# Kernel optimization log

Measured on AMD Instinct MI355X. Metric: run time of the kernel, lower is better.

The kernel has to match this reference:

```python
import jax, jax.numpy as jnp
import numpy as np

CANVAS = 28
MARGIN = 2
HALF = CANVAS / 2.0          # 14
SCALE = CANVAS / 2.0 - MARGIN  # 12
P = 2        # num_paths
SEG = 4      # final segments
T = 8        # curve samples per bezier segment
AA = 2       # 2x2 = 4 anti-alias subsamples per pixel


def _lin(x, w, b):
    return x @ w + b


def _render(cp, widths, alphas):
    """diffvg-style rasterizer.
    cp: [B,P,S,4,2] cubic bezier control points, widths/alphas: [B,P].
    Returns [B,1,H,W] image over white background (paths paint dark).
    """
    B = cp.shape[0]
    t = jnp.linspace(0.0, 1.0, T)
    mt = 1.0 - t
    basis = jnp.stack([mt**3, 3*mt**2*t, 3*mt*t**2, t**3], axis=1)  # [T,4]
    pts = jnp.einsum('tk,bpskd->bpstd', basis, cp)                   # [B,P,S,T,2]
    q = pts.reshape(B, P, SEG * T, 2)                                # polyline [B,P,M,2]

    # 2x2 subpixel sample grid over the canvas
    Nf = CANVAS * AA
    c = (jnp.arange(Nf, dtype=jnp.float32) + 0.5) / AA               # fine coords
    sy, sx = jnp.meshgrid(c, c, indexing='ij')
    s = jnp.stack([sx.ravel(), sy.ravel()], axis=-1)                 # [Ns,2] (x,y)

    # stroke coverage: distance from each sample to nearest curve sample
    qq = jnp.sum(q * q, axis=-1)                                     # [B,P,M]
    ss = jnp.sum(s * s, axis=-1)                                     # [Ns]
    cr = jnp.einsum('bpmd,nd->bpmn', q, s)                           # [B,P,M,Ns]
    d2 = jnp.maximum(qq[..., None] + ss - 2.0 * cr, 0.0)
    dist = jnp.sqrt(jnp.min(d2, axis=2))                             # [B,P,Ns]
    stroke = jnp.clip(widths[..., None] * 0.5 + 0.5 - dist, 0.0, 1.0)

    # fill coverage: even-odd crossing number on the closed polyline
    qn = jnp.roll(q, -1, axis=2)
    x0, y0 = q[..., 0], q[..., 1]
    x1, y1 = qn[..., 0], qn[..., 1]
    syf, sxf = s[:, 1], s[:, 0]
    crossing_band = (y0[..., None] > syf) != (y1[..., None] > syf)   # [B,P,M,Ns]
    te = (syf - y0[..., None]) / (y1[..., None] - y0[..., None] + 1e-8)
    xint = x0[..., None] + te * (x1 - x0)[..., None]
    ncross = jnp.sum((crossing_band & (sxf < xint)).astype(jnp.int32), axis=2)
    inside = (ncross % 2).astype(dist.dtype)                         # [B,P,Ns]

    cov = jnp.maximum(inside, stroke)
    img = jnp.prod(1.0 - alphas[..., None] * cov, axis=1)            # composite over paths, bg=1
    img = img.reshape(B, CANVAS, AA, CANVAS, AA).mean(axis=(2, 4))   # AA resolve
    return img[:, None]                                              # [B,1,H,W]


def setup_inputs() -> dict:
    key = jax.random.key(0)
    ks = jax.random.split(key, 16)
    def W(k, i, o):
        return jax.random.normal(k, (i, o), jnp.float32) / np.sqrt(i).astype(np.float32)
    B = 128
    return {
        'x': jax.random.uniform(ks[0], (B, 1, 28, 28), jnp.float32),
        'eps': jax.random.normal(ks[1], (B, 64), jnp.float32),
        'enc_w1': W(ks[2], 784, 256), 'enc_b1': jnp.zeros((256,), jnp.float32),
        'enc_w2': W(ks[3], 256, 256), 'enc_b2': jnp.zeros((256,), jnp.float32),
        'mu_w': W(ks[4], 256, 64), 'mu_b': jnp.zeros((64,), jnp.float32),
        'lv_w': W(ks[5], 256, 64), 'lv_b': jnp.zeros((64,), jnp.float32),
        'dec_w1': W(ks[6], 64, 512), 'dec_b1': jnp.zeros((512,), jnp.float32),
        'dec_w2': W(ks[7], 512, 512), 'dec_b2': jnp.zeros((512,), jnp.float32),
        'cp_w': W(ks[8], 512, 28), 'cp_b': jnp.zeros((28,), jnp.float32),
        'ref_w1': W(ks[9], 92, 512), 'ref_b1': jnp.zeros((512,), jnp.float32),
        'ref_w2': W(ks[10], 512, 52), 'ref_b2': jnp.zeros((52,), jnp.float32),
        'wd_w': W(ks[11], 512, 2), 'wd_b': jnp.zeros((2,), jnp.float32),
        'al_w': W(ks[12], 512, 2), 'al_b': jnp.zeros((2,), jnp.float32),
    }


def reference(x, eps, enc_w1, enc_b1, enc_w2, enc_b2, mu_w, mu_b, lv_w, lv_b,
              dec_w1, dec_b1, dec_w2, dec_b2, cp_w, cp_b,
              ref_w1, ref_b1, ref_w2, ref_b2, wd_w, wd_b, al_w, al_b):
    B = x.shape[0]
    # encoder
    h = jax.nn.leaky_relu(_lin(x.reshape(B, -1), enc_w1, enc_b1), 0.2)
    h = jax.nn.leaky_relu(_lin(h, enc_w2, enc_b2), 0.2)
    mu = _lin(h, mu_w, mu_b)
    logvar = _lin(h, lv_w, lv_b)
    z = mu + eps * jnp.exp(0.5 * logvar)
    # hierarchical decoder
    h2 = jax.nn.selu(_lin(jax.nn.selu(_lin(z, dec_w1, dec_b1)), dec_w2, dec_b2))
    coarse = jnp.tanh(_lin(h2, cp_w, cp_b)).reshape(B, P, 7, 2) * SCALE + HALF
    pts_norm = (coarse - HALF) / SCALE
    h_in = jnp.concatenate([z, pts_norm.reshape(B, -1)], axis=-1)
    refined = jnp.tanh(_lin(jax.nn.selu(_lin(h_in, ref_w1, ref_b1)), ref_w2, ref_b2))
    points = refined.reshape(B, P, 13, 2) * SCALE + HALF
    seg_idx = 3 * jnp.arange(SEG)[:, None] + jnp.arange(4)[None, :]  # [S,4]
    control_points = points[:, :, seg_idx, :]                         # [B,P,S,4,2]
    widths = jax.nn.sigmoid(_lin(h2, wd_w, wd_b)) * 2.0 + 1.0
    alphas = jax.nn.sigmoid(_lin(h2, al_w, al_b))
    rendered = 1.0 - _render(control_points, widths, alphas)          # white digit on black
    return (rendered, mu, logvar, control_points, widths, alphas)
```

## Files before the change

kernel.cpp:

```cpp
#include <hip/hip_runtime.h>
#include <math.h>


#define O_MU  100352
#define O_LV  108544
#define O_CP  116736
#define O_WD  124928
#define O_AL  125184

#define W_H1   0
#define W_HE   32768
#define W_MUT  65536
#define W_LVT  73728
#define W_D1   81920
#define W_H2   147456
#define W_PN   212992
#define W_R1   216576
#define W_PT   282112
#define W_WA   288768

__device__ __forceinline__ float leaky(float x) { return x >= 0.f ? x : 0.2f * x; }
__device__ __forceinline__ float seluf(float x) {
    const float s = 1.0507009873554805f, a = 1.6732632423543772f;
    return x > 0.f ? s * x : s * (a * expm1f(x));
}
__device__ __forceinline__ float sigm(float x) { return 1.f / (1.f + expf(-x)); }

__global__ __launch_bounds__(512)
void enc1_k(const float* __restrict__ x, const float* __restrict__ w,
            const float* __restrict__ b, float* __restrict__ outT) {
    __shared__ float part[8][64];
    const int j = blockIdx.x >> 1, h = blockIdx.x & 1;
    const int tid = threadIdx.x, lane = tid & 63, ks = tid >> 6;
    const int r = h * 64 + lane;
    const float* __restrict__ xr = x + r * 784;
    float acc = 0.f;
    const int k0 = ks * 98;
#pragma unroll 7
    for (int i = 0; i < 98; i++)
        acc = fmaf(xr[k0 + i], w[(k0 + i) * 256 + j], acc);
    part[ks][lane] = acc;
    __syncthreads();
    if (tid < 64) {
        float s = b[j];
#pragma unroll
        for (int q = 0; q < 8; q++) s += part[q][tid];
        outT[j * 128 + h * 64 + tid] = leaky(s);
    }
}

__global__ __launch_bounds__(512)
void enc2_k(const float* __restrict__ inT, const float* __restrict__ w,
            const float* __restrict__ b, float* __restrict__ outT) {
    __shared__ float part[8][64];
    const int j = blockIdx.x >> 1, h = blockIdx.x & 1;
    const int tid = threadIdx.x, lane = tid & 63, ks = tid >> 6;
    const int r = h * 64 + lane;
    float acc = 0.f;
    const int k0 = ks * 32;
#pragma unroll 8
    for (int i = 0; i < 32; i++)
        acc = fmaf(inT[(k0 + i) * 128 + r], w[(k0 + i) * 256 + j], acc);
    part[ks][lane] = acc;
    __syncthreads();
    if (tid < 64) {
        float s = b[j];
#pragma unroll
        for (int q = 0; q < 8; q++) s += part[q][tid];
        outT[j * 128 + h * 64 + tid] = leaky(s);
    }
}

__global__ __launch_bounds__(512)
void mulv_k(const float* __restrict__ heT,
            const float* __restrict__ mu_w, const float* __restrict__ mu_b,
            const float* __restrict__ lv_w, const float* __restrict__ lv_b,
            float* __restrict__ muT, float* __restrict__ lvT,
            float* __restrict__ out) {
    __shared__ float part[8][64];
    const int meta = blockIdx.x >> 1, h = blockIdx.x & 1;
    const int head = meta >> 6, col = meta & 63;
    const float* __restrict__ w = head ? lv_w : mu_w;
    const int tid = threadIdx.x, lane = tid & 63, ks = tid >> 6;
    const int r = h * 64 + lane;
    float acc = 0.f;
    const int k0 = ks * 32;
#pragma unroll 8
    for (int i = 0; i < 32; i++)
        acc = fmaf(heT[(k0 + i) * 128 + r], w[(k0 + i) * 64 + col], acc);
    part[ks][lane] = acc;
    __syncthreads();
    if (tid < 64) {
        float s = (head ? lv_b : mu_b)[col];
#pragma unroll
        for (int q = 0; q < 8; q++) s += part[q][tid];
        const int rr = h * 64 + tid;
        (head ? lvT : muT)[col * 128 + rr] = s;
        out[(head ? O_LV : O_MU) + rr * 64 + col] = s;
    }
}

__global__ __launch_bounds__(512)
void dec1_k(const float* __restrict__ muT, const float* __restrict__ lvT,
            const float* __restrict__ eps, const float* __restrict__ w,
            const float* __restrict__ b, float* __restrict__ outT) {
    __shared__ float part[8][2][64];
    const int j0 = (blockIdx.x >> 1) * 2, h = blockIdx.x & 1;
    const int tid = threadIdx.x, lane = tid & 63, ks = tid >> 6;
    const int r = h * 64 + lane;
    float a0 = 0.f, a1 = 0.f;
    const int k0 = ks * 8;
#pragma unroll
    for (int i = 0; i < 8; i++) {
        const int k = k0 + i;
        float zv = fmaf(eps[r * 64 + k], expf(0.5f * lvT[k * 128 + r]), muT[k * 128 + r]);
        a0 = fmaf(zv, w[k * 512 + j0],     a0);
        a1 = fmaf(zv, w[k * 512 + j0 + 1], a1);
    }
    part[ks][0][lane] = a0; part[ks][1][lane] = a1;
    __syncthreads();
    if (tid < 128) {
        const int c = tid >> 6, ll = tid & 63;
        float s = b[j0 + c];
#pragma unroll
        for (int q = 0; q < 8; q++) s += part[q][c][ll];
        outT[(j0 + c) * 128 + h * 64 + ll] = seluf(s);
    }
}

__global__ __launch_bounds__(512)
void dec2_k(const float* __restrict__ inT, const float* __restrict__ w,
            const float* __restrict__ b, float* __restrict__ outT) {
    __shared__ float part[8][2][64];
    const int j0 = (blockIdx.x >> 1) * 2, h = blockIdx.x & 1;
    const int tid = threadIdx.x, lane = tid & 63, ks = tid >> 6;
    const int r = h * 64 + lane;
    float a0 = 0.f, a1 = 0.f;
    const int k0 = ks * 64;
#pragma unroll 4
    for (int i = 0; i < 64; i++) {
        const float v = inT[(k0 + i) * 128 + r];
        a0 = fmaf(v, w[(k0 + i) * 512 + j0],     a0);
        a1 = fmaf(v, w[(k0 + i) * 512 + j0 + 1], a1);
    }
    part[ks][0][lane] = a0; part[ks][1][lane] = a1;
    __syncthreads();
    if (tid < 128) {
        const int c = tid >> 6, ll = tid & 63;
        float s = b[j0 + c];
#pragma unroll
        for (int q = 0; q < 8; q++) s += part[q][c][ll];
        outT[(j0 + c) * 128 + h * 64 + ll] = seluf(s);
    }
}

__global__ __launch_bounds__(512)
void heads_k(const float* __restrict__ h2T,
             const float* __restrict__ cp_w, const float* __restrict__ cp_b,
             const float* __restrict__ wd_w, const float* __restrict__ wd_b,
             const float* __restrict__ al_w, const float* __restrict__ al_b,
             float* __restrict__ pnT, float* __restrict__ waT,
             float* __restrict__ out) {
    __shared__ float part[8][64];
    const int j = blockIdx.x >> 1, h = blockIdx.x & 1;
    const float* __restrict__ w; int ldw, col;
    if (j < 28)      { w = cp_w; ldw = 28; col = j; }
    else if (j < 30) { w = wd_w; ldw = 2;  col = j - 28; }
    else             { w = al_w; ldw = 2;  col = j - 30; }
    const int tid = threadIdx.x, lane = tid & 63, ks = tid >> 6;
    const int r = h * 64 + lane;
    float acc = 0.f;
    const int k0 = ks * 64;
#pragma unroll 8
    for (int i = 0; i < 64; i++)
        acc = fmaf(h2T[(k0 + i) * 128 + r], w[(k0 + i) * ldw + col], acc);
    part[ks][lane] = acc;
    __syncthreads();
    if (tid < 64) {
        float s = 0.f;
#pragma unroll
        for (int q = 0; q < 8; q++) s += part[q][tid];
        const int rr = h * 64 + tid;
        if (j < 28) {
            pnT[j * 128 + rr] = tanhf(s + cp_b[col]);
        } else if (j < 30) {
            float v = fmaf(sigm(s + wd_b[col]), 2.f, 1.f);
            out[O_WD + rr * 2 + col] = v; waT[col * 128 + rr] = v;
        } else {
            float v = sigm(s + al_b[col]);
            out[O_AL + rr * 2 + col] = v; waT[(2 + col) * 128 + rr] = v;
        }
    }
}

__global__ __launch_bounds__(512)
void ref1_k(const float* __restrict__ muT, const float* __restrict__ lvT,
            const float* __restrict__ eps, const float* __restrict__ pnT,
            const float* __restrict__ w, const float* __restrict__ b,
            float* __restrict__ outT) {
    __shared__ float part[8][2][64];
    const int j0 = (blockIdx.x >> 1) * 2, h = blockIdx.x & 1;
    const int tid = threadIdx.x, lane = tid & 63, ks = tid >> 6;
    const int r = h * 64 + lane;
    float a0 = 0.f, a1 = 0.f;
#pragma unroll
    for (int i = 0; i < 12; i++) {
        const int k = ks * 12 + i;
        if (k < 92) {
            float v = (k < 64)
                ? fmaf(eps[r * 64 + k], expf(0.5f * lvT[k * 128 + r]), muT[k * 128 + r])
                : pnT[(k - 64) * 128 + r];
            a0 = fmaf(v, w[k * 512 + j0],     a0);
            a1 = fmaf(v, w[k * 512 + j0 + 1], a1);
        }
    }
    part[ks][0][lane] = a0; part[ks][1][lane] = a1;
    __syncthreads();
    if (tid < 128) {
        const int c = tid >> 6, ll = tid & 63;
        float s = b[j0 + c];
#pragma unroll
        for (int q = 0; q < 8; q++) s += part[q][c][ll];
        outT[(j0 + c) * 128 + h * 64 + ll] = seluf(s);
    }
}

__global__ __launch_bounds__(512)
void ref2_k(const float* __restrict__ r1T, const float* __restrict__ w,
            const float* __restrict__ b, float* __restrict__ PT) {
    __shared__ float part[8][64];
    const int j = blockIdx.x >> 1, h = blockIdx.x & 1;
    const int tid = threadIdx.x, lane = tid & 63, ks = tid >> 6;
    const int r = h * 64 + lane;
    float acc = 0.f;
    const int k0 = ks * 64;
#pragma unroll 8
    for (int i = 0; i < 64; i++)
        acc = fmaf(r1T[(k0 + i) * 128 + r], w[(k0 + i) * 52 + j], acc);
    part[ks][lane] = acc;
    __syncthreads();
    if (tid < 64) {
        float s = b[j];
#pragma unroll
        for (int q = 0; q < 8; q++) s += part[q][tid];
        PT[j * 128 + h * 64 + tid] = fmaf(tanhf(s), 12.f, 14.f);
    }
}

__global__ __launch_bounds__(512)
void raster_k(const float* __restrict__ PT, const float* __restrict__ waT,
              float* __restrict__ out) {
    __shared__ float sP[56];
    __shared__ float sWA[4];
    __shared__ float sQ[128];
    const int bid = blockIdx.x;
    const int row = bid / 7, chunk = bid - row * 7;
    const int tid = threadIdx.x;
    if (tid < 52) sP[tid] = PT[tid * 128 + row];
    if (tid >= 64 && tid < 68) sWA[tid - 64] = waT[(tid - 64) * 128 + row];
    __syncthreads();
    if (chunk == 0 && tid < 64) {
        const int idx = tid, p = idx >> 5, rest = idx & 31;
        const int s = rest >> 3, kk = (rest >> 1) & 3, d = idx & 1;
        out[O_CP + row * 64 + idx] = sP[p * 26 + (3 * s + kk) * 2 + d];
    }
    if (tid < 128) {
        const int idx = tid, p = idx >> 6, s = (idx >> 4) & 3, ti = (idx >> 1) & 7, d = idx & 1;
        const float t = (float)ti / 7.0f, mt = 1.0f - t;
        const float c0 = mt * mt * mt, c1 = 3.f * mt * mt * t;
        const float c2 = 3.f * mt * t * t, c3 = t * t * t;
        const float* base = sP + p * 26 + 6 * s + d;
        sQ[idx] = c0 * base[0] + c1 * base[2] + c2 * base[4] + c3 * base[6];
    }
    __syncthreads();
    if (tid < 448) {
        const int pixel = chunk * 112 + (tid >> 2), sub = tid & 3;
        const int py = pixel / 28, px = pixel - py * 28;
        const float sy = ((float)(2 * py + (sub >> 1)) + 0.5f) * 0.5f;
        const float sx = ((float)(2 * px + (sub & 1)) + 0.5f) * 0.5f;
        const float2* __restrict__ sQ2 = (const float2*)sQ;
        float img = 1.0f;
#pragma unroll
        for (int p = 0; p < 2; p++) {
            float dmin2 = 1e30f;
            int cnt = 0;
            float2 cur = sQ2[p * 32];
            bool bp = cur.y > sy;
#pragma unroll
            for (int m = 0; m < 32; m++) {
                float2 nxt = sQ2[p * 32 + ((m + 1) & 31)];
                float dx = sx - cur.x;
                float dy = sy - cur.y;
                dmin2 = fminf(dmin2, fmaf(dx, dx, dy * dy));
                bool bn = nxt.y > sy;
                float den = nxt.y - cur.y + 1e-8f;
                float lhs = dx * den;
                float rhs = dy * (nxt.x - cur.x);
                if ((bp != bn) && ((lhs < rhs) == (den > 0.0f))) cnt++;
                cur = nxt;
                bp = bn;
            }
            float dist = sqrtf(dmin2);
            float stroke = fminf(fmaxf(fmaf(sWA[p], 0.5f, 0.5f) - dist, 0.f), 1.f);
            float cov = fmaxf((float)(cnt & 1), stroke);
            img *= fmaf(-sWA[2 + p], cov, 1.0f);
        }
        img += __shfl_xor(img, 1);
        img += __shfl_xor(img, 2);
        if (sub == 0) out[row * 784 + pixel] = 1.0f - 0.25f * img;
    }
}

extern "C" void kernel_launch(void* const* d_in, const int* in_sizes, int n_in,
                              void* d_out, int out_size, void* d_ws, size_t ws_size,
                              hipStream_t stream) {
    const float* x      = (const float*)d_in[0];
    const float* eps    = (const float*)d_in[1];
    const float* enc_w1 = (const float*)d_in[2];
    const float* enc_b1 = (const float*)d_in[3];
    const float* enc_w2 = (const float*)d_in[4];
    const float* enc_b2 = (const float*)d_in[5];
    const float* mu_w   = (const float*)d_in[6];
    const float* mu_b   = (const float*)d_in[7];
    const float* lv_w   = (const float*)d_in[8];
    const float* lv_b   = (const float*)d_in[9];
    const float* dec_w1 = (const float*)d_in[10];
    const float* dec_b1 = (const float*)d_in[11];
    const float* dec_w2 = (const float*)d_in[12];
    const float* dec_b2 = (const float*)d_in[13];
    const float* cp_w   = (const float*)d_in[14];
    const float* cp_b   = (const float*)d_in[15];
    const float* ref_w1 = (const float*)d_in[16];
    const float* ref_b1 = (const float*)d_in[17];
    const float* ref_w2 = (const float*)d_in[18];
    const float* ref_b2 = (const float*)d_in[19];
    const float* wd_w   = (const float*)d_in[20];
    const float* wd_b   = (const float*)d_in[21];
    const float* al_w   = (const float*)d_in[22];
    const float* al_b   = (const float*)d_in[23];

    float* out = (float*)d_out;
    float* ws  = (float*)d_ws;

    enc1_k <<<512, 512, 0, stream>>>(x, enc_w1, enc_b1, ws + W_H1);
    enc2_k <<<512, 512, 0, stream>>>(ws + W_H1, enc_w2, enc_b2, ws + W_HE);
    mulv_k <<<256, 512, 0, stream>>>(ws + W_HE, mu_w, mu_b, lv_w, lv_b,
                                     ws + W_MUT, ws + W_LVT, out);
    dec1_k <<<512, 512, 0, stream>>>(ws + W_MUT, ws + W_LVT, eps,
                                     dec_w1, dec_b1, ws + W_D1);
    dec2_k <<<512, 512, 0, stream>>>(ws + W_D1, dec_w2, dec_b2, ws + W_H2);
    heads_k<<<64, 512, 0, stream>>>(ws + W_H2, cp_w, cp_b, wd_w, wd_b, al_w, al_b,
                                    ws + W_PN, ws + W_WA, out);
    ref1_k <<<512, 512, 0, stream>>>(ws + W_MUT, ws + W_LVT, eps, ws + W_PN,
                                     ref_w1, ref_b1, ws + W_R1);
    ref2_k <<<104, 512, 0, stream>>>(ws + W_R1, ref_w2, ref_b2, ws + W_PT);
    raster_k<<<896, 512, 0, stream>>>(ws + W_PT, ws + W_WA, out);
}
```

Baseline: 190.0 us.

## Fuse whole VAE pipeline into one cooperative kernel with grid syncs

Replaces the nine separate layer and raster launches with a single cooperative kernel of 256 blocks that uses grid-wide syncs between layers. It also splits the refine layer so the z-dependent part is computed while the heads run, and it touches later-layer weights early to warm the cache. The aim is to remove per-launch overhead and inter-kernel gaps. In exchange it runs fewer blocks per stage and adds the cost of each grid barrier.

Result: slower. 469.8 us (+147.3%).

```diff
diff --git a/kernel.cpp b/kernel.cpp
--- a/kernel.cpp
+++ b/kernel.cpp
@@ -1,5 +1,8 @@
 #include <hip/hip_runtime.h>
+#include <hip/hip_cooperative_groups.h>
 #include <math.h>
+
+namespace cg = cooperative_groups;
 
 
 #define O_MU  100352
@@ -15,9 +18,10 @@
 #define W_D1   81920
 #define W_H2   147456
 #define W_PN   212992
-#define W_R1   216576
-#define W_PT   282112
-#define W_WA   288768
+#define W_R1Z  216576
+#define W_R1   282112
+#define W_PT   347648
+#define W_WA   354304
 
 __device__ __forceinline__ float leaky(float x) { return x >= 0.f ? x : 0.2f * x; }
 __device__ __forceinline__ float seluf(float x) {
@@ -27,287 +31,300 @@
 __device__ __forceinline__ float sigm(float x) { return 1.f / (1.f + expf(-x)); }
 
 __global__ __launch_bounds__(512)
-void enc1_k(const float* __restrict__ x, const float* __restrict__ w,
-            const float* __restrict__ b, float* __restrict__ outT) {
-    __shared__ float part[8][64];
-    const int j = blockIdx.x >> 1, h = blockIdx.x & 1;
-    const int tid = threadIdx.x, lane = tid & 63, ks = tid >> 6;
-    const int r = h * 64 + lane;
-    const float* __restrict__ xr = x + r * 784;
-    float acc = 0.f;
-    const int k0 = ks * 98;
-#pragma unroll 7
-    for (int i = 0; i < 98; i++)
-        acc = fmaf(xr[k0 + i], w[(k0 + i) * 256 + j], acc);
-    part[ks][lane] = acc;
-    __syncthreads();
-    if (tid < 64) {
-        float s = b[j];
-#pragma unroll
-        for (int q = 0; q < 8; q++) s += part[q][tid];
-        outT[j * 128 + h * 64 + tid] = leaky(s);
-    }
-}
-
-__global__ __launch_bounds__(512)
-void enc2_k(const float* __restrict__ inT, const float* __restrict__ w,
-            const float* __restrict__ b, float* __restrict__ outT) {
-    __shared__ float part[8][64];
-    const int j = blockIdx.x >> 1, h = blockIdx.x & 1;
-    const int tid = threadIdx.x, lane = tid & 63, ks = tid >> 6;
-    const int r = h * 64 + lane;
-    float acc = 0.f;
-    const int k0 = ks * 32;
-#pragma unroll 8
-    for (int i = 0; i < 32; i++)
-        acc = fmaf(inT[(k0 + i) * 128 + r], w[(k0 + i) * 256 + j], acc);
-    part[ks][lane] = acc;
-    __syncthreads();
-    if (tid < 64) {
-        float s = b[j];
-#pragma unroll
-        for (int q = 0; q < 8; q++) s += part[q][tid];
-        outT[j * 128 + h * 64 + tid] = leaky(s);
-    }
-}
-
-__global__ __launch_bounds__(512)
-void mulv_k(const float* __restrict__ heT,
-            const float* __restrict__ mu_w, const float* __restrict__ mu_b,
-            const float* __restrict__ lv_w, const float* __restrict__ lv_b,
-            float* __restrict__ muT, float* __restrict__ lvT,
-            float* __restrict__ out) {
-    __shared__ float part[8][64];
-    const int meta = blockIdx.x >> 1, h = blockIdx.x & 1;
-    const int head = meta >> 6, col = meta & 63;
-    const float* __restrict__ w = head ? lv_w : mu_w;
-    const int tid = threadIdx.x, lane = tid & 63, ks = tid >> 6;
-    const int r = h * 64 + lane;
-    float acc = 0.f;
-    const int k0 = ks * 32;
-#pragma unroll 8
-    for (int i = 0; i < 32; i++)
-        acc = fmaf(heT[(k0 + i) * 128 + r], w[(k0 + i) * 64 + col], acc);
-    part[ks][lane] = acc;
-    __syncthreads();
-    if (tid < 64) {
-        float s = (head ? lv_b : mu_b)[col];
-#pragma unroll
-        for (int q = 0; q < 8; q++) s += part[q][tid];
-        const int rr = h * 64 + tid;
-        (head ? lvT : muT)[col * 128 + rr] = s;
-        out[(head ? O_LV : O_MU) + rr * 64 + col] = s;
-    }
-}
-
-__global__ __launch_bounds__(512)
-void dec1_k(const float* __restrict__ muT, const float* __restrict__ lvT,
-            const float* __restrict__ eps, const float* __restrict__ w,
-            const float* __restrict__ b, float* __restrict__ outT) {
-    __shared__ float part[8][2][64];
-    const int j0 = (blockIdx.x >> 1) * 2, h = blockIdx.x & 1;
-    const int tid = threadIdx.x, lane = tid & 63, ks = tid >> 6;
-    const int r = h * 64 + lane;
-    float a0 = 0.f, a1 = 0.f;
-    const int k0 = ks * 8;
-#pragma unroll
-    for (int i = 0; i < 8; i++) {
-        const int k = k0 + i;
-        float zv = fmaf(eps[r * 64 + k], expf(0.5f * lvT[k * 128 + r]), muT[k * 128 + r]);
-        a0 = fmaf(zv, w[k * 512 + j0],     a0);
-        a1 = fmaf(zv, w[k * 512 + j0 + 1], a1);
-    }
-    part[ks][0][lane] = a0; part[ks][1][lane] = a1;
-    __syncthreads();
-    if (tid < 128) {
-        const int c = tid >> 6, ll = tid & 63;
-        float s = b[j0 + c];
-#pragma unroll
-        for (int q = 0; q < 8; q++) s += part[q][c][ll];
-        outT[(j0 + c) * 128 + h * 64 + ll] = seluf(s);
-    }
-}
-
-__global__ __launch_bounds__(512)
-void dec2_k(const float* __restrict__ inT, const float* __restrict__ w,
-            const float* __restrict__ b, float* __restrict__ outT) {
-    __shared__ float part[8][2][64];
-    const int j0 = (blockIdx.x >> 1) * 2, h = blockIdx.x & 1;
-    const int tid = threadIdx.x, lane = tid & 63, ks = tid >> 6;
-    const int r = h * 64 + lane;
-    float a0 = 0.f, a1 = 0.f;
-    const int k0 = ks * 64;
-#pragma unroll 4
-    for (int i = 0; i < 64; i++) {
-        const float v = inT[(k0 + i) * 128 + r];
-        a0 = fmaf(v, w[(k0 + i) * 512 + j0],     a0);
-        a1 = fmaf(v, w[(k0 + i) * 512 + j0 + 1], a1);
-    }
-    part[ks][0][lane] = a0; part[ks][1][lane] = a1;
-    __syncthreads();
-    if (tid < 128) {
-        const int c = tid >> 6, ll = tid & 63;
-        float s = b[j0 + c];
-#pragma unroll
-        for (int q = 0; q < 8; q++) s += part[q][c][ll];
-        outT[(j0 + c) * 128 + h * 64 + ll] = seluf(s);
-    }
-}
-
-__global__ __launch_bounds__(512)
-void heads_k(const float* __restrict__ h2T,
-             const float* __restrict__ cp_w, const float* __restrict__ cp_b,
-             const float* __restrict__ wd_w, const float* __restrict__ wd_b,
-             const float* __restrict__ al_w, const float* __restrict__ al_b,
-             float* __restrict__ pnT, float* __restrict__ waT,
-             float* __restrict__ out) {
-    __shared__ float part[8][64];
-    const int j = blockIdx.x >> 1, h = blockIdx.x & 1;
-    const float* __restrict__ w; int ldw, col;
-    if (j < 28)      { w = cp_w; ldw = 28; col = j; }
-    else if (j < 30) { w = wd_w; ldw = 2;  col = j - 28; }
-    else             { w = al_w; ldw = 2;  col = j - 30; }
-    const int tid = threadIdx.x, lane = tid & 63, ks = tid >> 6;
-    const int r = h * 64 + lane;
-    float acc = 0.f;
-    const int k0 = ks * 64;
-#pragma unroll 8
-    for (int i = 0; i < 64; i++)
-        acc = fmaf(h2T[(k0 + i) * 128 + r], w[(k0 + i) * ldw + col], acc);
-    part[ks][lane] = acc;
-    __syncthreads();
-    if (tid < 64) {
-        float s = 0.f;
-#pragma unroll
-        for (int q = 0; q < 8; q++) s += part[q][tid];
-        const int rr = h * 64 + tid;
-        if (j < 28) {
-            pnT[j * 128 + rr] = tanhf(s + cp_b[col]);
-        } else if (j < 30) {
-            float v = fmaf(sigm(s + wd_b[col]), 2.f, 1.f);
-            out[O_WD + rr * 2 + col] = v; waT[col * 128 + rr] = v;
-        } else {
-            float v = sigm(s + al_b[col]);
-            out[O_AL + rr * 2 + col] = v; waT[(2 + col) * 128 + rr] = v;
-        }
-    }
-}
-
-__global__ __launch_bounds__(512)
-void ref1_k(const float* __restrict__ muT, const float* __restrict__ lvT,
-            const float* __restrict__ eps, const float* __restrict__ pnT,
-            const float* __restrict__ w, const float* __restrict__ b,
-            float* __restrict__ outT) {
-    __shared__ float part[8][2][64];
-    const int j0 = (blockIdx.x >> 1) * 2, h = blockIdx.x & 1;
-    const int tid = threadIdx.x, lane = tid & 63, ks = tid >> 6;
-    const int r = h * 64 + lane;
-    float a0 = 0.f, a1 = 0.f;
-#pragma unroll
-    for (int i = 0; i < 12; i++) {
-        const int k = ks * 12 + i;
-        if (k < 92) {
-            float v = (k < 64)
-                ? fmaf(eps[r * 64 + k], expf(0.5f * lvT[k * 128 + r]), muT[k * 128 + r])
-                : pnT[(k - 64) * 128 + r];
-            a0 = fmaf(v, w[k * 512 + j0],     a0);
-            a1 = fmaf(v, w[k * 512 + j0 + 1], a1);
-        }
-    }
-    part[ks][0][lane] = a0; part[ks][1][lane] = a1;
-    __syncthreads();
-    if (tid < 128) {
-        const int c = tid >> 6, ll = tid & 63;
-        float s = b[j0 + c];
-#pragma unroll
-        for (int q = 0; q < 8; q++) s += part[q][c][ll];
-        outT[(j0 + c) * 128 + h * 64 + ll] = seluf(s);
-    }
-}
-
-__global__ __launch_bounds__(512)
-void ref2_k(const float* __restrict__ r1T, const float* __restrict__ w,
-            const float* __restrict__ b, float* __restrict__ PT) {
-    __shared__ float part[8][64];
-    const int j = blockIdx.x >> 1, h = blockIdx.x & 1;
-    const int tid = threadIdx.x, lane = tid & 63, ks = tid >> 6;
-    const int r = h * 64 + lane;
-    float acc = 0.f;
-    const int k0 = ks * 64;
-#pragma unroll 8
-    for (int i = 0; i < 64; i++)
-        acc = fmaf(r1T[(k0 + i) * 128 + r], w[(k0 + i) * 52 + j], acc);
-    part[ks][lane] = acc;
-    __syncthreads();
-    if (tid < 64) {
-        float s = b[j];
-#pragma unroll
-        for (int q = 0; q < 8; q++) s += part[q][tid];
-        PT[j * 128 + h * 64 + tid] = fmaf(tanhf(s), 12.f, 14.f);
-    }
-}
-
-__global__ __launch_bounds__(512)
-void raster_k(const float* __restrict__ PT, const float* __restrict__ waT,
-              float* __restrict__ out) {
+void vae_coop(const float* __restrict__ x, const float* __restrict__ eps,
+              const float* __restrict__ enc_w1, const float* __restrict__ enc_b1,
+              const float* __restrict__ enc_w2, const float* __restrict__ enc_b2,
+              const float* __restrict__ mu_w, const float* __restrict__ mu_b,
+              const float* __restrict__ lv_w, const float* __restrict__ lv_b,
+              const float* __restrict__ dec_w1, const float* __restrict__ dec_b1,
+              const float* __restrict__ dec_w2, const float* __restrict__ dec_b2,
+              const float* __restrict__ cp_w, const float* __restrict__ cp_b,
+              const float* __restrict__ ref_w1, const float* __restrict__ ref_b1,
+              const float* __restrict__ ref_w2, const float* __restrict__ ref_b2,
+              const float* __restrict__ wd_w, const float* __restrict__ wd_b,
+              const float* __restrict__ al_w, const float* __restrict__ al_b,
+              float* __restrict__ out, float* __restrict__ ws) {
+    cg::grid_group grid = cg::this_grid();
+    __shared__ float part[4][2][128];
     __shared__ float sP[56];
     __shared__ float sWA[4];
     __shared__ float sQ[128];
-    const int bid = blockIdx.x;
-    const int row = bid / 7, chunk = bid - row * 7;
+
+    const int b = blockIdx.x;
+    const int L = (b & 7) * 32 + (b >> 3);
     const int tid = threadIdx.x;
-    if (tid < 52) sP[tid] = PT[tid * 128 + row];
-    if (tid >= 64 && tid < 68) sWA[tid - 64] = waT[(tid - 64) * 128 + row];
-    __syncthreads();
-    if (chunk == 0 && tid < 64) {
-        const int idx = tid, p = idx >> 5, rest = idx & 31;
-        const int s = rest >> 3, kk = (rest >> 1) & 3, d = idx & 1;
-        out[O_CP + row * 64 + idx] = sP[p * 26 + (3 * s + kk) * 2 + d];
-    }
+    const int r = tid & 127;
+    const int ks = tid >> 7;
+
+    float* const h1T  = ws + W_H1;
+    float* const heT  = ws + W_HE;
+    float* const muT  = ws + W_MUT;
+    float* const lvT  = ws + W_LVT;
+    float* const d1T  = ws + W_D1;
+    float* const h2T  = ws + W_H2;
+    float* const pnT  = ws + W_PN;
+    float* const r1zT = ws + W_R1Z;
+    float* const r1T  = ws + W_R1;
+    float* const PT   = ws + W_PT;
+    float* const waT  = ws + W_WA;
+
+    float pf = 0.f;
+    {
+        const int j0 = 2 * L;
+        pf += dec_w2[tid * 512 + j0];
+        if (tid < 92)  pf += ref_w1[tid * 512 + j0];
+        if (tid < 64)  pf += dec_w1[tid * 512 + j0];
+        if (tid < 256) pf += enc_w2[tid * 256 + L];
+        if (b < 128 && tid < 256)
+            pf += (b >= 64 ? lv_w : mu_w)[tid * 64 + (b & 63)];
+        if (b < 28)    pf += cp_w[tid * 28 + b];
+        if (b < 52)    pf += ref_w2[tid * 52 + b];
+    }
+
+    {
+        const float* __restrict__ xr = x + r * 784;
+        const int k0 = ks * 196;
+        float acc = 0.f;
+#pragma unroll 4
+        for (int i = 0; i < 196; i++)
+            acc = fmaf(xr[k0 + i], enc_w1[(k0 + i) * 256 + L], acc);
+        asm volatile("" :: "v"(pf));
+        part[ks][0][r] = acc;
+    }
+    __syncthreads();
     if (tid < 128) {
-        const int idx = tid, p = idx >> 6, s = (idx >> 4) & 3, ti = (idx >> 1) & 7, d = idx & 1;
-        const float t = (float)ti / 7.0f, mt = 1.0f - t;
-        const float c0 = mt * mt * mt, c1 = 3.f * mt * mt * t;
-        const float c2 = 3.f * mt * t * t, c3 = t * t * t;
-        const float* base = sP + p * 26 + 6 * s + d;
-        sQ[idx] = c0 * base[0] + c1 * base[2] + c2 * base[4] + c3 * base[6];
-    }
-    __syncthreads();
-    if (tid < 448) {
-        const int pixel = chunk * 112 + (tid >> 2), sub = tid & 3;
-        const int py = pixel / 28, px = pixel - py * 28;
-        const float sy = ((float)(2 * py + (sub >> 1)) + 0.5f) * 0.5f;
-        const float sx = ((float)(2 * px + (sub & 1)) + 0.5f) * 0.5f;
+        float s = enc_b1[L];
+#pragma unroll
+        for (int q = 0; q < 4; q++) s += part[q][0][tid];
+        h1T[L * 128 + tid] = leaky(s);
+    }
+    grid.sync();
+
+    {
+        const int k0 = ks * 64;
+        float acc = 0.f;
+#pragma unroll 8
+        for (int i = 0; i < 64; i++)
+            acc = fmaf(h1T[(k0 + i) * 128 + r], enc_w2[(k0 + i) * 256 + L], acc);
+        part[ks][0][r] = acc;
+    }
+    __syncthreads();
+    if (tid < 128) {
+        float s = enc_b2[L];
+#pragma unroll
+        for (int q = 0; q < 4; q++) s += part[q][0][tid];
+        heT[L * 128 + tid] = leaky(s);
+    }
+    grid.sync();
+
+    if (b < 128) {
+        const int head = b >> 6, col = b & 63;
+        const float* __restrict__ w = head ? lv_w : mu_w;
+        const int k0 = ks * 64;
+        float acc = 0.f;
+#pragma unroll 8
+        for (int i = 0; i < 64; i++)
+            acc = fmaf(heT[(k0 + i) * 128 + r], w[(k0 + i) * 64 + col], acc);
+        part[ks][0][r] = acc;
+        __syncthreads();
+        if (tid < 128) {
+            float s = (head ? lv_b : mu_b)[col];
+#pragma unroll
+            for (int q = 0; q < 4; q++) s += part[q][0][tid];
+            (head ? lvT : muT)[col * 128 + tid] = s;
+            out[(head ? O_LV : O_MU) + tid * 64 + col] = s;
+        }
+    }
+    grid.sync();
+
+    {
+        const int j0 = 2 * L, k0 = ks * 16;
+        float a0 = 0.f, a1 = 0.f;
+#pragma unroll
+        for (int i = 0; i < 16; i++) {
+            const int k = k0 + i;
+            float zv = fmaf(eps[r * 64 + k], expf(0.5f * lvT[k * 128 + r]), muT[k * 128 + r]);
+            a0 = fmaf(zv, dec_w1[k * 512 + j0],     a0);
+            a1 = fmaf(zv, dec_w1[k * 512 + j0 + 1], a1);
+        }
+        part[ks][0][r] = a0; part[ks][1][r] = a1;
+    }
+    __syncthreads();
+    if (tid < 256) {
+        const int c = tid >> 7, ll = tid & 127;
+        float s = dec_b1[2 * L + c];
+#pragma unroll
+        for (int q = 0; q < 4; q++) s += part[q][c][ll];
+        d1T[(2 * L + c) * 128 + ll] = seluf(s);
+    }
+    grid.sync();
+
+    {
+        const int j0 = 2 * L, k0 = ks * 128;
+        float a0 = 0.f, a1 = 0.f;
+#pragma unroll 4
+        for (int i = 0; i < 128; i++) {
+            const float v = d1T[(k0 + i) * 128 + r];
+            a0 = fmaf(v, dec_w2[(k0 + i) * 512 + j0],     a0);
+            a1 = fmaf(v, dec_w2[(k0 + i) * 512 + j0 + 1], a1);
+        }
+        part[ks][0][r] = a0; part[ks][1][r] = a1;
+    }
+    __syncthreads();
+    if (tid < 256) {
+        const int c = tid >> 7, ll = tid & 127;
+        float s = dec_b2[2 * L + c];
+#pragma unroll
+        for (int q = 0; q < 4; q++) s += part[q][c][ll];
+        h2T[(2 * L + c) * 128 + ll] = seluf(s);
+    }
+    grid.sync();
+
+    {
+        const int j0 = 2 * L, k0 = ks * 16;
+        float a0 = 0.f, a1 = 0.f;
+#pragma unroll
+        for (int i = 0; i < 16; i++) {
+            const int k = k0 + i;
+            float zv = fmaf(eps[r * 64 + k], expf(0.5f * lvT[k * 128 + r]), muT[k * 128 + r]);
+            a0 = fmaf(zv, ref_w1[k * 512 + j0],     a0);
+            a1 = fmaf(zv, ref_w1[k * 512 + j0 + 1], a1);
+        }
+        part[ks][0][r] = a0; part[ks][1][r] = a1;
+    }
+    __syncthreads();
+    if (tid < 256) {
+        const int c = tid >> 7, ll = tid & 127;
+        float s = 0.f;
+#pragma unroll
+        for (int q = 0; q < 4; q++) s += part[q][c][ll];
+        r1zT[(2 * L + c) * 128 + ll] = s;
+    }
+    __syncthreads();
+    if (b < 32) {
+        const float* __restrict__ w; int ldw, col;
+        if (b < 28)      { w = cp_w; ldw = 28; col = b; }
+        else if (b < 30) { w = wd_w; ldw = 2;  col = b - 28; }
+        else             { w = al_w; ldw = 2;  col = b - 30; }
+        const int k0 = ks * 128;
+        float acc = 0.f;
+#pragma unroll 4
+        for (int i = 0; i < 128; i++)
+            acc = fmaf(h2T[(k0 + i) * 128 + r], w[(k0 + i) * ldw + col], acc);
+        part[ks][0][r] = acc;
+        __syncthreads();
+        if (tid < 128) {
+            float s = 0.f;
+#pragma unroll
+            for (int q = 0; q < 4; q++) s += part[q][0][tid];
+            if (b < 28) {
+                pnT[b * 128 + tid] = tanhf(s + cp_b[col]);
+            } else if (b < 30) {
+                float v = fmaf(sigm(s + wd_b[col]), 2.f, 1.f);
+                out[O_WD + tid * 2 + col] = v; waT[col * 128 + tid] = v;
+            } else {
+                float v = sigm(s + al_b[col]);
+                out[O_AL + tid * 2 + col] = v; waT[(2 + col) * 128 + tid] = v;
+            }
+        }
+    }
+    grid.sync();
+
+    {
+        const int j0 = 2 * L, k0 = 64 + ks * 7;
+        float a0 = 0.f, a1 = 0.f;
+#pragma unroll
+        for (int i = 0; i < 7; i++) {
+            const int k = k0 + i;
+            const float v = pnT[(k - 64) * 128 + r];
+            a0 = fmaf(v, ref_w1[k * 512 + j0],     a0);
+            a1 = fmaf(v, ref_w1[k * 512 + j0 + 1], a1);
+        }
+        part[ks][0][r] = a0; part[ks][1][r] = a1;
+    }
+    __syncthreads();
+    if (tid < 256) {
+        const int c = tid >> 7, ll = tid & 127;
+        float s = ref_b1[2 * L + c] + r1zT[(2 * L + c) * 128 + ll];
+#pragma unroll
+        for (int q = 0; q < 4; q++) s += part[q][c][ll];
+        r1T[(2 * L + c) * 128 + ll] = seluf(s);
+    }
+    grid.sync();
+
+    if (b < 52) {
+        const int k0 = ks * 128;
+        float acc = 0.f;
+#pragma unroll 4
+        for (int i = 0; i < 128; i++)
+            acc = fmaf(r1T[(k0 + i) * 128 + r], ref_w2[(k0 + i) * 52 + b], acc);
+        part[ks][0][r] = acc;
+        __syncthreads();
+        if (tid < 128) {
+            float s = ref_b2[b];
+#pragma unroll
+            for (int q = 0; q < 4; q++) s += part[q][0][tid];
+            PT[b * 128 + tid] = fmaf(tanhf(s), 12.f, 14.f);
+        }
+    }
+    grid.sync();
+
+    {
+        const int row = b >> 1, half = b & 1;
+        if (tid < 52) sP[tid] = PT[tid * 128 + row];
+        if (tid >= 64 && tid < 68) sWA[tid - 64] = waT[(tid - 64) * 128 + row];
+        __syncthreads();
+        if (half == 0 && tid < 64) {
+            const int idx = tid, p = idx >> 5, rest = idx & 31;
+            const int s = rest >> 3, kk = (rest >> 1) & 3, d = idx & 1;
+            out[O_CP + row * 64 + idx] = sP[p * 26 + (3 * s + kk) * 2 + d];
+        }
+        if (tid < 128) {
+            const int idx = tid, p = idx >> 6, s = (idx >> 4) & 3, ti = (idx >> 1) & 7, d = idx & 1;
+            const float t = (float)ti / 7.0f, mt = 1.0f - t;
+            const float c0 = mt * mt * mt, c1 = 3.f * mt * mt * t;
+            const float c2 = 3.f * mt * t * t, c3 = t * t * t;
+            const float* base = sP + p * 26 + 6 * s + d;
+            sQ[idx] = c0 * base[0] + c1 * base[2] + c2 * base[4] + c3 * base[6];
+        }
+        __syncthreads();
         const float2* __restrict__ sQ2 = (const float2*)sQ;
-        float img = 1.0f;
-#pragma unroll
-        for (int p = 0; p < 2; p++) {
-            float dmin2 = 1e30f;
-            int cnt = 0;
-            float2 cur = sQ2[p * 32];
-            bool bp = cur.y > sy;
-#pragma unroll
-            for (int m = 0; m < 32; m++) {
-                float2 nxt = sQ2[p * 32 + ((m + 1) & 31)];
-                float dx = sx - cur.x;
-                float dy = sy - cur.y;
-                dmin2 = fminf(dmin2, fmaf(dx, dx, dy * dy));
-                bool bn = nxt.y > sy;
-                float den = nxt.y - cur.y + 1e-8f;
-                float lhs = dx * den;
-                float rhs = dy * (nxt.x - cur.x);
-                if ((bp != bn) && ((lhs < rhs) == (den > 0.0f))) cnt++;
-                cur = nxt;
-                bp = bn;
+        for (int u = tid; u < 1568; u += 512) {
+            const int pixel = half * 392 + (u >> 2);
+            const int sub = u & 3;
+            const int py = pixel / 28, px = pixel - py * 28;
+            const float sy = ((float)(2 * py + (sub >> 1)) + 0.5f) * 0.5f;
+            const float sx = ((float)(2 * px + (sub & 1)) + 0.5f) * 0.5f;
+            float img = 1.0f;
+#pragma unroll
+            for (int p = 0; p < 2; p++) {
+                float dmin2 = 1e30f;
+                int cnt = 0;
+                float2 cur = sQ2[p * 32];
+                bool bp = cur.y > sy;
+#pragma unroll
+                for (int m = 0; m < 32; m++) {
+                    float2 nxt = sQ2[p * 32 + ((m + 1) & 31)];
+                    float dx = sx - cur.x;
+                    float dy = sy - cur.y;
+                    dmin2 = fminf(dmin2, fmaf(dx, dx, dy * dy));
+                    bool bn = nxt.y > sy;
+                    float den = nxt.y - cur.y + 1e-8f;
+                    float lhs = dx * den;
+                    float rhs = dy * (nxt.x - cur.x);
+                    if ((bp != bn) && ((lhs < rhs) == (den > 0.0f))) cnt++;
+                    cur = nxt;
+                    bp = bn;
+                }
+                float dist = sqrtf(dmin2);
+                float stroke = fminf(fmaxf(fmaf(sWA[p], 0.5f, 0.5f) - dist, 0.f), 1.f);
+                float cov = fmaxf((float)(cnt & 1), stroke);
+                img *= fmaf(-sWA[2 + p], cov, 1.0f);
             }
-            float dist = sqrtf(dmin2);
-            float stroke = fminf(fmaxf(fmaf(sWA[p], 0.5f, 0.5f) - dist, 0.f), 1.f);
-            float cov = fmaxf((float)(cnt & 1), stroke);
-            img *= fmaf(-sWA[2 + p], cov, 1.0f);
-        }
-        img += __shfl_xor(img, 1);
-        img += __shfl_xor(img, 2);
-        if (sub == 0) out[row * 784 + pixel] = 1.0f - 0.25f * img;
+            img += __shfl_xor(img, 1);
+            img += __shfl_xor(img, 2);
+            if (sub == 0) out[row * 784 + pixel] = 1.0f - 0.25f * img;
+        }
     }
 }
 
@@ -342,17 +359,15 @@
     float* out = (float*)d_out;
     float* ws  = (float*)d_ws;
 
-    enc1_k <<<512, 512, 0, stream>>>(x, enc_w1, enc_b1, ws + W_H1);
-    enc2_k <<<512, 512, 0, stream>>>(ws + W_H1, enc_w2, enc_b2, ws + W_HE);
-    mulv_k <<<256, 512, 0, stream>>>(ws + W_HE, mu_w, mu_b, lv_w, lv_b,
-                                     ws + W_MUT, ws + W_LVT, out);
-    dec1_k <<<512, 512, 0, stream>>>(ws + W_MUT, ws + W_LVT, eps,
-                                     dec_w1, dec_b1, ws + W_D1);
-    dec2_k <<<512, 512, 0, stream>>>(ws + W_D1, dec_w2, dec_b2, ws + W_H2);
-    heads_k<<<64, 512, 0, stream>>>(ws + W_H2, cp_w, cp_b, wd_w, wd_b, al_w, al_b,
-                                    ws + W_PN, ws + W_WA, out);
-    ref1_k <<<512, 512, 0, stream>>>(ws + W_MUT, ws + W_LVT, eps, ws + W_PN,
-                                     ref_w1, ref_b1, ws + W_R1);
-    ref2_k <<<104, 512, 0, stream>>>(ws + W_R1, ref_w2, ref_b2, ws + W_PT);
-    raster_k<<<896, 512, 0, stream>>>(ws + W_PT, ws + W_WA, out);
+    void* args[] = {
+        (void*)&x, (void*)&eps,
+        (void*)&enc_w1, (void*)&enc_b1, (void*)&enc_w2, (void*)&enc_b2,
+        (void*)&mu_w, (void*)&mu_b, (void*)&lv_w, (void*)&lv_b,
+        (void*)&dec_w1, (void*)&dec_b1, (void*)&dec_w2, (void*)&dec_b2,
+        (void*)&cp_w, (void*)&cp_b, (void*)&ref_w1, (void*)&ref_b1,
+        (void*)&ref_w2, (void*)&ref_b2, (void*)&wd_w, (void*)&wd_b,
+        (void*)&al_w, (void*)&al_b, (void*)&out, (void*)&ws
+    };
+    hipLaunchCooperativeKernel((void*)vae_coop, dim3(256), dim3(512),
+                               args, 0, stream);
 }
```

## Fuse encoder-mid and decoder-tail layers into per-row kernels, cutting launches

Applied to the files above, without the earlier changes.

Replaces enc2, mu/logvar, dec1 with one per-row mid kernel and heads, ref1, ref2, raster with one per-row tail kernel (two blocks per row, each rendering half the image). Activations stay in shared memory across layers, so launch count drops from nine to four and intermediate global round-trips disappear. In exchange, each tail block redundantly recomputes the small MLP layers for its row, and the fused kernels launch fewer blocks (128 and 256), so there is less parallelism per layer.

New measurement: 229.6 us. 20.9% more time.

```diff
diff --git a/kernel.cpp b/kernel.cpp
--- a/kernel.cpp
+++ b/kernel.cpp
@@ -9,15 +9,10 @@
 #define O_AL  125184
 
 #define W_H1   0
-#define W_HE   32768
-#define W_MUT  65536
-#define W_LVT  73728
-#define W_D1   81920
-#define W_H2   147456
-#define W_PN   212992
-#define W_R1   216576
-#define W_PT   282112
-#define W_WA   288768
+#define W_MUT  32768
+#define W_LVT  40960
+#define W_D1   49152
+#define W_H2   114688
 
 __device__ __forceinline__ float leaky(float x) { return x >= 0.f ? x : 0.2f * x; }
 __device__ __forceinline__ float seluf(float x) {
@@ -50,81 +45,57 @@
 }
 
 __global__ __launch_bounds__(512)
-void enc2_k(const float* __restrict__ inT, const float* __restrict__ w,
-            const float* __restrict__ b, float* __restrict__ outT) {
-    __shared__ float part[8][64];
-    const int j = blockIdx.x >> 1, h = blockIdx.x & 1;
-    const int tid = threadIdx.x, lane = tid & 63, ks = tid >> 6;
-    const int r = h * 64 + lane;
-    float acc = 0.f;
-    const int k0 = ks * 32;
+void mid_k(const float* __restrict__ h1T,
+           const float* __restrict__ enc_w2, const float* __restrict__ enc_b2,
+           const float* __restrict__ mu_w, const float* __restrict__ mu_b,
+           const float* __restrict__ lv_w, const float* __restrict__ lv_b,
+           const float* __restrict__ eps,
+           const float* __restrict__ dec_w1, const float* __restrict__ dec_b1,
+           float* __restrict__ muT, float* __restrict__ lvT,
+           float* __restrict__ d1T, float* __restrict__ out) {
+    __shared__ float sh1[256], she[256], sml[128], sz[64];
+    const int row = blockIdx.x, tid = threadIdx.x;
+    if (tid < 256) sh1[tid] = h1T[tid * 128 + row];
+    __syncthreads();
+    {
+        const int o = tid >> 1, g = tid & 1;
+        float acc = 0.f;
+        const int k0 = g * 128;
 #pragma unroll 8
-    for (int i = 0; i < 32; i++)
-        acc = fmaf(inT[(k0 + i) * 128 + r], w[(k0 + i) * 256 + j], acc);
-    part[ks][lane] = acc;
-    __syncthreads();
-    if (tid < 64) {
-        float s = b[j];
-#pragma unroll
-        for (int q = 0; q < 8; q++) s += part[q][tid];
-        outT[j * 128 + h * 64 + tid] = leaky(s);
-    }
-}
-
-__global__ __launch_bounds__(512)
-void mulv_k(const float* __restrict__ heT,
-            const float* __restrict__ mu_w, const float* __restrict__ mu_b,
-            const float* __restrict__ lv_w, const float* __restrict__ lv_b,
-            float* __restrict__ muT, float* __restrict__ lvT,
-            float* __restrict__ out) {
-    __shared__ float part[8][64];
-    const int meta = blockIdx.x >> 1, h = blockIdx.x & 1;
-    const int head = meta >> 6, col = meta & 63;
-    const float* __restrict__ w = head ? lv_w : mu_w;
-    const int tid = threadIdx.x, lane = tid & 63, ks = tid >> 6;
-    const int r = h * 64 + lane;
-    float acc = 0.f;
-    const int k0 = ks * 32;
+        for (int i = 0; i < 128; i++)
+            acc = fmaf(sh1[k0 + i], enc_w2[(k0 + i) * 256 + o], acc);
+        acc += __shfl_xor(acc, 1);
+        if (g == 0) she[o] = leaky(acc + enc_b2[o]);
+    }
+    __syncthreads();
+    {
+        const int o = tid >> 2, g = tid & 3;
+        const float* __restrict__ w = (o < 64) ? mu_w : lv_w;
+        const int col = o & 63;
+        float acc = 0.f;
+        const int k0 = g * 64;
 #pragma unroll 8
-    for (int i = 0; i < 32; i++)
-        acc = fmaf(heT[(k0 + i) * 128 + r], w[(k0 + i) * 64 + col], acc);
-    part[ks][lane] = acc;
-    __syncthreads();
-    if (tid < 64) {
-        float s = (head ? lv_b : mu_b)[col];
-#pragma unroll
-        for (int q = 0; q < 8; q++) s += part[q][tid];
-        const int rr = h * 64 + tid;
-        (head ? lvT : muT)[col * 128 + rr] = s;
-        out[(head ? O_LV : O_MU) + rr * 64 + col] = s;
-    }
-}
-
-__global__ __launch_bounds__(512)
-void dec1_k(const float* __restrict__ muT, const float* __restrict__ lvT,
-            const float* __restrict__ eps, const float* __restrict__ w,
-            const float* __restrict__ b, float* __restrict__ outT) {
-    __shared__ float part[8][2][64];
-    const int j0 = (blockIdx.x >> 1) * 2, h = blockIdx.x & 1;
-    const int tid = threadIdx.x, lane = tid & 63, ks = tid >> 6;
-    const int r = h * 64 + lane;
-    float a0 = 0.f, a1 = 0.f;
-    const int k0 = ks * 8;
-#pragma unroll
-    for (int i = 0; i < 8; i++) {
-        const int k = k0 + i;
-        float zv = fmaf(eps[r * 64 + k], expf(0.5f * lvT[k * 128 + r]), muT[k * 128 + r]);
-        a0 = fmaf(zv, w[k * 512 + j0],     a0);
-        a1 = fmaf(zv, w[k * 512 + j0 + 1], a1);
-    }
-    part[ks][0][lane] = a0; part[ks][1][lane] = a1;
-    __syncthreads();
-    if (tid < 128) {
-        const int c = tid >> 6, ll = tid & 63;
-        float s = b[j0 + c];
-#pragma unroll
-        for (int q = 0; q < 8; q++) s += part[q][c][ll];
-        outT[(j0 + c) * 128 + h * 64 + ll] = seluf(s);
+        for (int i = 0; i < 64; i++)
+            acc = fmaf(she[k0 + i], w[(k0 + i) * 64 + col], acc);
+        acc += __shfl_xor(acc, 1);
+        acc += __shfl_xor(acc, 2);
+        if (g == 0) {
+            float s = acc + ((o < 64) ? mu_b : lv_b)[col];
+            sml[o] = s;
+            ((o < 64) ? muT : lvT)[col * 128 + row] = s;
+            out[((o < 64) ? O_MU : O_LV) + row * 64 + col] = s;
+        }
+    }
+    __syncthreads();
+    if (tid < 64)
+        sz[tid] = fmaf(eps[row * 64 + tid], expf(0.5f * sml[64 + tid]), sml[tid]);
+    __syncthreads();
+    {
+        float acc = 0.f;
+#pragma unroll 8
+        for (int k = 0; k < 64; k++)
+            acc = fmaf(sz[k], dec_w1[k * 512 + tid], acc);
+        d1T[tid * 128 + row] = seluf(acc + dec_b1[tid]);
     }
 }
 
@@ -155,111 +126,81 @@
 }
 
 __global__ __launch_bounds__(512)
-void heads_k(const float* __restrict__ h2T,
-             const float* __restrict__ cp_w, const float* __restrict__ cp_b,
-             const float* __restrict__ wd_w, const float* __restrict__ wd_b,
-             const float* __restrict__ al_w, const float* __restrict__ al_b,
-             float* __restrict__ pnT, float* __restrict__ waT,
-             float* __restrict__ out) {
-    __shared__ float part[8][64];
-    const int j = blockIdx.x >> 1, h = blockIdx.x & 1;
-    const float* __restrict__ w; int ldw, col;
-    if (j < 28)      { w = cp_w; ldw = 28; col = j; }
-    else if (j < 30) { w = wd_w; ldw = 2;  col = j - 28; }
-    else             { w = al_w; ldw = 2;  col = j - 30; }
-    const int tid = threadIdx.x, lane = tid & 63, ks = tid >> 6;
-    const int r = h * 64 + lane;
-    float acc = 0.f;
-    const int k0 = ks * 64;
-#pragma unroll 8
-    for (int i = 0; i < 64; i++)
-        acc = fmaf(h2T[(k0 + i) * 128 + r], w[(k0 + i) * ldw + col], acc);
-    part[ks][lane] = acc;
-    __syncthreads();
-    if (tid < 64) {
-        float s = 0.f;
-#pragma unroll
-        for (int q = 0; q < 8; q++) s += part[q][tid];
-        const int rr = h * 64 + tid;
-        if (j < 28) {
-            pnT[j * 128 + rr] = tanhf(s + cp_b[col]);
-        } else if (j < 30) {
-            float v = fmaf(sigm(s + wd_b[col]), 2.f, 1.f);
-            out[O_WD + rr * 2 + col] = v; waT[col * 128 + rr] = v;
-        } else {
-            float v = sigm(s + al_b[col]);
-            out[O_AL + rr * 2 + col] = v; waT[(2 + col) * 128 + rr] = v;
-        }
-    }
-}
-
-__global__ __launch_bounds__(512)
-void ref1_k(const float* __restrict__ muT, const float* __restrict__ lvT,
-            const float* __restrict__ eps, const float* __restrict__ pnT,
-            const float* __restrict__ w, const float* __restrict__ b,
-            float* __restrict__ outT) {
-    __shared__ float part[8][2][64];
-    const int j0 = (blockIdx.x >> 1) * 2, h = blockIdx.x & 1;
-    const int tid = threadIdx.x, lane = tid & 63, ks = tid >> 6;
-    const int r = h * 64 + lane;
-    float a0 = 0.f, a1 = 0.f;
-#pragma unroll
-    for (int i = 0; i < 12; i++) {
-        const int k = ks * 12 + i;
-        if (k < 92) {
-            float v = (k < 64)
-                ? fmaf(eps[r * 64 + k], expf(0.5f * lvT[k * 128 + r]), muT[k * 128 + r])
-                : pnT[(k - 64) * 128 + r];
-            a0 = fmaf(v, w[k * 512 + j0],     a0);
-            a1 = fmaf(v, w[k * 512 + j0 + 1], a1);
-        }
-    }
-    part[ks][0][lane] = a0; part[ks][1][lane] = a1;
-    __syncthreads();
-    if (tid < 128) {
-        const int c = tid >> 6, ll = tid & 63;
-        float s = b[j0 + c];
-#pragma unroll
-        for (int q = 0; q < 8; q++) s += part[q][c][ll];
-        outT[(j0 + c) * 128 + h * 64 + ll] = seluf(s);
-    }
-}
-
-__global__ __launch_bounds__(512)
-void ref2_k(const float* __restrict__ r1T, const float* __restrict__ w,
-            const float* __restrict__ b, float* __restrict__ PT) {
-    __shared__ float part[8][64];
-    const int j = blockIdx.x >> 1, h = blockIdx.x & 1;
-    const int tid = threadIdx.x, lane = tid & 63, ks = tid >> 6;
-    const int r = h * 64 + lane;
-    float acc = 0.f;
-    const int k0 = ks * 64;
-#pragma unroll 8
-    for (int i = 0; i < 64; i++)
-        acc = fmaf(r1T[(k0 + i) * 128 + r], w[(k0 + i) * 52 + j], acc);
-    part[ks][lane] = acc;
-    __syncthreads();
-    if (tid < 64) {
-        float s = b[j];
-#pragma unroll
-        for (int q = 0; q < 8; q++) s += part[q][tid];
-        PT[j * 128 + h * 64 + tid] = fmaf(tanhf(s), 12.f, 14.f);
-    }
-}
-
-__global__ __launch_bounds__(512)
-void raster_k(const float* __restrict__ PT, const float* __restrict__ waT,
-              float* __restrict__ out) {
+void tail_k(const float* __restrict__ h2T, const float* __restrict__ muT,
+            const float* __restrict__ lvT, const float* __restrict__ eps,
+            const float* __restrict__ cp_w, const float* __restrict__ cp_b,
+            const float* __restrict__ wd_w, const float* __restrict__ wd_b,
+            const float* __restrict__ al_w, const float* __restrict__ al_b,
+            const float* __restrict__ ref_w1, const float* __restrict__ ref_b1,
+            const float* __restrict__ ref_w2, const float* __restrict__ ref_b2,
+            float* __restrict__ out) {
+    __shared__ float sh2[512];
+    __shared__ float sIn[96];
+    __shared__ float sR1[512];
     __shared__ float sP[56];
     __shared__ float sWA[4];
     __shared__ float sQ[128];
-    const int bid = blockIdx.x;
-    const int row = bid / 7, chunk = bid - row * 7;
+    const int row = blockIdx.x >> 1, half = blockIdx.x & 1;
     const int tid = threadIdx.x;
-    if (tid < 52) sP[tid] = PT[tid * 128 + row];
-    if (tid >= 64 && tid < 68) sWA[tid - 64] = waT[(tid - 64) * 128 + row];
-    __syncthreads();
-    if (chunk == 0 && tid < 64) {
+
+    sh2[tid] = h2T[tid * 128 + row];
+    if (tid < 64) {
+        float mu = muT[tid * 128 + row], lv = lvT[tid * 128 + row];
+        sIn[tid] = fmaf(eps[row * 64 + tid], expf(0.5f * lv), mu);
+    }
+    __syncthreads();
+
+    {
+        const int o = tid >> 4, g = tid & 15;
+        const float* __restrict__ w; int ldw, col;
+        if (o < 28)      { w = cp_w; ldw = 28; col = o; }
+        else if (o < 30) { w = wd_w; ldw = 2;  col = o - 28; }
+        else             { w = al_w; ldw = 2;  col = o - 30; }
+        float acc = 0.f;
+        for (int k = g; k < 512; k += 16) acc = fmaf(sh2[k], w[k * ldw + col], acc);
+        acc += __shfl_xor(acc, 1);
+        acc += __shfl_xor(acc, 2);
+        acc += __shfl_xor(acc, 4);
+        acc += __shfl_xor(acc, 8);
+        if (g == 0) {
+            if (o < 28) {
+                sIn[64 + o] = tanhf(acc + cp_b[col]);
+            } else if (o < 30) {
+                float v = fmaf(sigm(acc + wd_b[col]), 2.f, 1.f);
+                if (half == 0) out[O_WD + row * 2 + col] = v;
+                sWA[col] = v;
+            } else {
+                float v = sigm(acc + al_b[col]);
+                if (half == 0) out[O_AL + row * 2 + col] = v;
+                sWA[2 + col] = v;
+            }
+        }
+    }
+    __syncthreads();
+
+    {
+        float acc = 0.f;
+#pragma unroll 4
+        for (int k = 0; k < 92; k++)
+            acc = fmaf(sIn[k], ref_w1[k * 512 + tid], acc);
+        sR1[tid] = seluf(acc + ref_b1[tid]);
+    }
+    __syncthreads();
+
+    {
+        const int o = tid >> 3, g = tid & 7;
+        float acc = 0.f;
+        if (o < 52)
+            for (int k = g; k < 512; k += 8) acc = fmaf(sR1[k], ref_w2[k * 52 + o], acc);
+        acc += __shfl_xor(acc, 1);
+        acc += __shfl_xor(acc, 2);
+        acc += __shfl_xor(acc, 4);
+        if (g == 0 && o < 52)
+            sP[o] = fmaf(tanhf(acc + ref_b2[o]), 12.f, 14.f);
+    }
+    __syncthreads();
+
+    if (half == 0 && tid < 64) {
         const int idx = tid, p = idx >> 5, rest = idx & 31;
         const int s = rest >> 3, kk = (rest >> 1) & 3, d = idx & 1;
         out[O_CP + row * 64 + idx] = sP[p * 26 + (3 * s + kk) * 2 + d];
@@ -273,12 +214,14 @@
         sQ[idx] = c0 * base[0] + c1 * base[2] + c2 * base[4] + c3 * base[6];
     }
     __syncthreads();
-    if (tid < 448) {
-        const int pixel = chunk * 112 + (tid >> 2), sub = tid & 3;
+
+    const float2* __restrict__ sQ2 = (const float2*)sQ;
+    for (int u = tid; u < 1568; u += 512) {
+        const int pixel = half * 392 + (u >> 2);
+        const int sub = u & 3;
         const int py = pixel / 28, px = pixel - py * 28;
         const float sy = ((float)(2 * py + (sub >> 1)) + 0.5f) * 0.5f;
         const float sx = ((float)(2 * px + (sub & 1)) + 0.5f) * 0.5f;
-        const float2* __restrict__ sQ2 = (const float2*)sQ;
         float img = 1.0f;
 #pragma unroll
         for (int p = 0; p < 2; p++) {
@@ -342,17 +285,13 @@
     float* out = (float*)d_out;
     float* ws  = (float*)d_ws;
 
-    enc1_k <<<512, 512, 0, stream>>>(x, enc_w1, enc_b1, ws + W_H1);
-    enc2_k <<<512, 512, 0, stream>>>(ws + W_H1, enc_w2, enc_b2, ws + W_HE);
-    mulv_k <<<256, 512, 0, stream>>>(ws + W_HE, mu_w, mu_b, lv_w, lv_b,
-                                     ws + W_MUT, ws + W_LVT, out);
-    dec1_k <<<512, 512, 0, stream>>>(ws + W_MUT, ws + W_LVT, eps,
-                                     dec_w1, dec_b1, ws + W_D1);
-    dec2_k <<<512, 512, 0, stream>>>(ws + W_D1, dec_w2, dec_b2, ws + W_H2);
-    heads_k<<<64, 512, 0, stream>>>(ws + W_H2, cp_w, cp_b, wd_w, wd_b, al_w, al_b,
-                                    ws + W_PN, ws + W_WA, out);
-    ref1_k <<<512, 512, 0, stream>>>(ws + W_MUT, ws + W_LVT, eps, ws + W_PN,
-                                     ref_w1, ref_b1, ws + W_R1);
-    ref2_k <<<104, 512, 0, stream>>>(ws + W_R1, ref_w2, ref_b2, ws + W_PT);
-    raster_k<<<896, 512, 0, stream>>>(ws + W_PT, ws + W_WA, out);
-}
+    enc1_k<<<512, 512, 0, stream>>>(x, enc_w1, enc_b1, ws + W_H1);
+    mid_k <<<128, 512, 0, stream>>>(ws + W_H1, enc_w2, enc_b2,
+                                    mu_w, mu_b, lv_w, lv_b, eps,
+                                    dec_w1, dec_b1,
+                                    ws + W_MUT, ws + W_LVT, ws + W_D1, out);
+    dec2_k<<<512, 512, 0, stream>>>(ws + W_D1, dec_w2, dec_b2, ws + W_H2);
+    tail_k<<<256, 512, 0, stream>>>(ws + W_H2, ws + W_MUT, ws + W_LVT, eps,
+                                    cp_w, cp_b, wd_w, wd_b, al_w, al_b,
+                                    ref_w1, ref_b1, ref_w2, ref_b2, out);
+}
```
